# Kernel tuning notes

Hardware: AMD Instinct MI355X
Metric: run time of the kernel (lower is better)

## Reference

```python
import jax, jax.numpy as jnp
import numpy as np
import math

N_EMBD = 1024
N_HEAD = 16
BLOCK_SIZE = 2048
B, T = 4, 2048

def setup_inputs() -> dict:
    key = jax.random.key(0)
    ks = jax.random.split(key, 5)
    s = 0.02
    x = jax.random.normal(ks[0], (B, T, N_EMBD), dtype=jnp.float32)
    W_attn = jax.random.normal(ks[1], (N_EMBD, 3 * N_EMBD), dtype=jnp.float32) * s
    b_attn = jnp.zeros((3 * N_EMBD,), dtype=jnp.float32)
    W_proj = jax.random.normal(ks[2], (N_EMBD, N_EMBD), dtype=jnp.float32) * s
    b_proj = jnp.zeros((N_EMBD,), dtype=jnp.float32)
    return {"x": x, "W_attn": W_attn, "b_attn": b_attn, "W_proj": W_proj, "b_proj": b_proj}

def reference(x, W_attn, b_attn, W_proj, b_proj):
    b, t, c = x.shape
    hd = c // N_HEAD  # head dim
    qkv = x @ W_attn + b_attn                      # [B,T,3C]
    q, k, v = jnp.split(qkv, 3, axis=-1)
    # [B,T,C] -> [B,H,T,hd]
    q = q.reshape(b, t, N_HEAD, hd).transpose(0, 2, 1, 3)
    k = k.reshape(b, t, N_HEAD, hd).transpose(0, 2, 1, 3)
    v = v.reshape(b, t, N_HEAD, hd).transpose(0, 2, 1, 3)
    att = jnp.einsum('bhqd,bhkd->bhqk', q, k) * (1.0 / math.sqrt(hd))
    causal = jnp.tril(jnp.ones((t, t), dtype=bool))
    att = jnp.where(causal[None, None], att, -jnp.inf)
    att = jax.nn.softmax(att, axis=-1)
    y = jnp.einsum('bhqk,bhkd->bhqd', att, v)      # [B,H,T,hd]
    y = y.transpose(0, 2, 1, 3).reshape(b, t, c)
    return y @ W_proj + b_proj
```

## Files before the change

kernel.cpp:

```cpp
#include <hip/hip_runtime.h>

typedef unsigned short u16;
typedef __bf16 bf16x8 __attribute__((ext_vector_type(8)));
typedef float    f32x4 __attribute__((ext_vector_type(4)));
typedef unsigned short u16x8 __attribute__((ext_vector_type(8)));

__device__ __forceinline__ float bf2f(u16 v){ return __uint_as_float(((unsigned int)v) << 16); }
__device__ __forceinline__ u16 f2bf(float f){
    unsigned int u = __float_as_uint(f);
    u += 0x7fffu + ((u >> 16) & 1u);
    return (u16)(u >> 16);
}
__device__ __forceinline__ u16 f2bf_t(float f){ return (u16)(__float_as_uint(f) >> 16); }
__device__ __forceinline__ unsigned pack_trunc(float hi, float lo){
    return __builtin_amdgcn_perm(__float_as_uint(hi), __float_as_uint(lo), 0x07060302);
}
__device__ __forceinline__ float exp2_fast(float x){
    float r; asm("v_exp_f32 %0, %1" : "=v"(r) : "v"(x)); return r;
}

__device__ __forceinline__ void glds16(const u16* gp, u16* lp){
    __builtin_amdgcn_global_load_lds((unsigned int __attribute__((address_space(1)))*)gp,
                                     (unsigned int __attribute__((address_space(3)))*)lp,
                                     16, 0, 0);
}

__device__ __forceinline__ int probe_f32(const u16* __restrict__ xp){
    u16 lo = xp[2 * (threadIdx.x & 63)];
    int e = (lo >> 7) & 0xff;
    bool bad = !(e == 0 || (e > 96 && e < 160));
    return __popcll(__ballot(bad)) > 16;
}

__global__ __launch_bounds__(256) void conv_x(const void* __restrict__ src, u16* __restrict__ dst,
                                              const u16* __restrict__ xprobe){
    const int isf32 = probe_f32(xprobe);
    size_t i = ((size_t)blockIdx.x * 256 + threadIdx.x) * 8;
    if (isf32){
        const float* p = (const float*)src + i;
        float4 a = *(const float4*)p, b = *(const float4*)(p + 4);
        u16x8 o = { f2bf(a.x), f2bf(a.y), f2bf(a.z), f2bf(a.w),
                    f2bf(b.x), f2bf(b.y), f2bf(b.z), f2bf(b.w) };
        *(u16x8*)(dst + i) = o;
    } else {
        *(u16x8*)(dst + i) = *(const u16x8*)((const u16*)src + i);
    }
}

__global__ __launch_bounds__(256) void transposeW(const void* __restrict__ in, u16* __restrict__ out,
                                                  int R, int C, const u16* __restrict__ xprobe){
    __shared__ u16 t[64][65];
    const int isf32 = probe_f32(xprobe);
    const int c0 = blockIdx.x * 64, r0 = blockIdx.y * 64;
    const int tx = threadIdx.x & 15, ty = threadIdx.x >> 4;
#pragma unroll
    for (int i = 0; i < 4; i++){
        int r = ty + i * 16;
        u16 a, b, c, d;
        if (isf32){
            float4 v = *(const float4*)((const float*)in + (size_t)(r0 + r) * C + c0 + tx * 4);
            a = f2bf(v.x); b = f2bf(v.y); c = f2bf(v.z); d = f2bf(v.w);
        } else {
            ushort4 v = *(const ushort4*)((const u16*)in + (size_t)(r0 + r) * C + c0 + tx * 4);
            a = v.x; b = v.y; c = v.z; d = v.w;
        }
        t[r][tx*4+0] = a; t[r][tx*4+1] = b; t[r][tx*4+2] = c; t[r][tx*4+3] = d;
    }
    __syncthreads();
#pragma unroll
    for (int i = 0; i < 4; i++){
        int oc = ty + i * 16;
        ushort4 v;
        v.x = t[tx*4+0][oc]; v.y = t[tx*4+1][oc]; v.z = t[tx*4+2][oc]; v.w = t[tx*4+3][oc];
        *(ushort4*)(out + (size_t)(c0 + oc) * R + r0 + tx * 4) = v;
    }
}

#define CTS 136
template<int MODE>
__global__ __launch_bounds__(256) void gemm128(
    const u16* __restrict__ A, const u16* __restrict__ Bt, const void* __restrict__ bias,
    void* __restrict__ C, u16* __restrict__ Cq, u16* __restrict__ Ck, u16* __restrict__ Cv,
    const u16* __restrict__ xprobe, int M, int N, int K)
{
    __shared__ u16 lds[17408];
    u16* Asm = lds;
    u16* Bsm = lds + 8192;
    u16* Ct  = lds;
    const int isf32 = probe_f32(xprobe);
    const int tid = threadIdx.x;
    const int wave = tid >> 6, lane = tid & 63;
    const int quad = lane >> 4, ml = lane & 15;

    const int nbx = gridDim.x;
    int flat = blockIdx.y * nbx + blockIdx.x;
    const int cpx = (nbx * gridDim.y) >> 3;
    flat = (flat & 7) * cpx + (flat >> 3);
    const int m_blk = (flat / nbx) * 128;
    const int n_blk = (flat % nbx) * 128;

    const int wm = (wave >> 1) * 64, wn = (wave & 1) * 64;
    const int srow = lane >> 3;
    const int sch  = lane & 7;

    f32x4 acc[4][4];
#pragma unroll
    for (int a = 0; a < 4; a++)
#pragma unroll
        for (int b = 0; b < 4; b++)
            acc[a][b] = (f32x4){0.f, 0.f, 0.f, 0.f};

    for (int k0 = 0; k0 < K; k0 += 64){
        __syncthreads();
#pragma unroll
        for (int i = 0; i < 4; i++){
            int row = wave * 32 + i * 8 + srow;
            int sc  = sch ^ (row & 7);
            glds16(A  + (size_t)(m_blk + row) * K + k0 + sc * 8, Asm + (wave * 32 + i * 8) * 64);
            glds16(Bt + (size_t)(n_blk + row) * K + k0 + sc * 8, Bsm + (wave * 32 + i * 8) * 64);
        }
        __syncthreads();
#pragma unroll
        for (int ks = 0; ks < 2; ks++){
            bf16x8 af[4], bfr[4];
#pragma unroll
            for (int mt = 0; mt < 4; mt++)
                af[mt]  = *(const bf16x8*)&Asm[(wm + mt * 16 + ml) * 64 + ((ks * 4 + quad) ^ (ml & 7)) * 8];
#pragma unroll
            for (int nt = 0; nt < 4; nt++)
                bfr[nt] = *(const bf16x8*)&Bsm[(wn + nt * 16 + ml) * 64 + ((ks * 4 + quad) ^ (ml & 7)) * 8];
#pragma unroll
            for (int mt = 0; mt < 4; mt++)
#pragma unroll
                for (int nt = 0; nt < 4; nt++)
                    acc[mt][nt] = __builtin_amdgcn_mfma_f32_16x16x32_bf16(af[mt], bfr[nt], acc[mt][nt], 0, 0, 0);
        }
    }
    __syncthreads();

    const float QSC = 0.18033688f;
    if (MODE == 0){
        const int which = n_blk >> 10;
        const int hbase = (n_blk >> 6) & 15;
        if (which < 2){
            const float sc = (which == 0) ? QSC : 1.0f;
#pragma unroll
            for (int nt = 0; nt < 4; nt++){
                int col = wn + nt * 16 + ml;
                float bv = isf32 ? ((const float*)bias)[n_blk + col] : bf2f(((const u16*)bias)[n_blk + col]);
#pragma unroll
                for (int mt = 0; mt < 4; mt++){
                    int row0 = wm + mt * 16 + quad * 4;
#pragma unroll
                    for (int r = 0; r < 4; r++)
                        Ct[(row0 + r) * CTS + col] = f2bf_t((acc[mt][nt][r] + bv) * sc);
                }
            }
            __syncthreads();
            u16* dst0 = (which == 0) ? Cq : Ck;
            const int b = m_blk >> 11, t0 = m_blk & 2047;
#pragma unroll
            for (int i = 0; i < 8; i++){
                int u = i * 256 + tid;
                int row = u >> 4, c8 = u & 15;
                int h = hbase + (c8 >> 3), d8 = (c8 & 7) * 8;
                u16x8 v = *(const u16x8*)&Ct[row * CTS + c8 * 8];
                *(u16x8*)&dst0[(((size_t)(b * 16 + h)) * 2048 + (t0 + row)) * 64 + d8] = v;
            }
        } else {
#pragma unroll
            for (int nt = 0; nt < 4; nt++){
                int col = wn + nt * 16 + ml;
                float bv = isf32 ? ((const float*)bias)[n_blk + col] : bf2f(((const u16*)bias)[n_blk + col]);
#pragma unroll
                for (int mt = 0; mt < 4; mt++){
                    int row0 = wm + mt * 16 + quad * 4;
                    uint2 pk;
                    pk.x = pack_trunc(acc[mt][nt][1] + bv, acc[mt][nt][0] + bv);
                    pk.y = pack_trunc(acc[mt][nt][3] + bv, acc[mt][nt][2] + bv);
                    *(uint2*)&Ct[col * CTS + row0] = pk;
                }
            }
            __syncthreads();
            const int b = m_blk >> 11, t0 = m_blk & 2047;
#pragma unroll
            for (int i = 0; i < 8; i++){
                int u = i * 256 + tid;
                int col = u >> 4, c8 = u & 15;
                int h = hbase + (col >> 6), d = col & 63;
                u16x8 v = *(const u16x8*)&Ct[col * CTS + c8 * 8];
                *(u16x8*)&Cv[(((size_t)(b * 16 + h)) * 64 + d) * 2048 + t0 + c8 * 8] = v;
            }
        }
    } else {
#pragma unroll
        for (int nt = 0; nt < 4; nt++){
            int col = n_blk + wn + nt * 16 + ml;
            float bv = isf32 ? ((const float*)bias)[col] : bf2f(((const u16*)bias)[col]);
#pragma unroll
            for (int mt = 0; mt < 4; mt++){
                float o0 = acc[mt][nt][0] + bv, o1 = acc[mt][nt][1] + bv;
                float o2 = acc[mt][nt][2] + bv, o3 = acc[mt][nt][3] + bv;
                int row0 = m_blk + wm + mt * 16 + quad * 4;
                if (isf32){
                    float* p = (float*)C + (size_t)row0 * N + col;
                    p[0] = o0; p[N] = o1; p[2*N] = o2; p[3*N] = o3;
                } else {
                    u16* p = (u16*)C + (size_t)row0 * N + col;
                    p[0] = f2bf(o0); p[N] = f2bf(o1); p[2*N] = f2bf(o2); p[3*N] = f2bf(o3);
                }
            }
        }
    }
}

#define PS 136
__global__ __launch_bounds__(256) void attn_kernel(
    const u16* __restrict__ Q, const u16* __restrict__ K, const u16* __restrict__ Vt,
    u16* __restrict__ Y)
{
    __shared__ u16 Ksm[128 * 64];
    __shared__ u16 Vsm[64 * 128];
    __shared__ u16 Psm[4][32 * PS];

    const int tid = threadIdx.x, wave = tid >> 6, lane = tid & 63;
    const int quad = lane >> 4, ml = lane & 15;
    const int flat = blockIdx.x;
    const int qb = 15 - (flat >> 6);
    const int rest = flat & 63;
    const int bh = ((rest & 7) << 3) | (rest >> 3);
    const int q0 = qb * 128;
    const size_t base = (size_t)bh * (2048 * 64);
    const float NEG = -1.0e30f;

    bf16x8 qf[2][2];
#pragma unroll
    for (int mt = 0; mt < 2; mt++)
#pragma unroll
        for (int ks = 0; ks < 2; ks++)
            qf[mt][ks] = *(const bf16x8*)(Q + base + (size_t)(q0 + mt * 64 + wave * 16 + ml) * 64 + ks * 32 + quad * 8);

    f32x4 acc[2][4];
#pragma unroll
    for (int mt = 0; mt < 2; mt++)
#pragma unroll
        for (int nt = 0; nt < 4; nt++) acc[mt][nt] = (f32x4){0.f, 0.f, 0.f, 0.f};
    float l[2][4];
#pragma unroll
    for (int mt = 0; mt < 2; mt++)
#pragma unroll
        for (int r = 0; r < 4; r++) l[mt][r] = 0.f;

    const int ntj = qb + 1;
    for (int j = 0; j < ntj; j++){
        const int j0 = j * 128;
        __syncthreads();
#pragma unroll
        for (int i = 0; i < 4; i++){
            int ub = i * 256 + wave * 64;
            int u = ub + lane;
            int row = u >> 3, cg = (lane & 7) ^ (row & 7);
            glds16(K + base + (size_t)(j0 + row) * 64 + cg * 8, Ksm + ub * 8);
            int d = u >> 4, vg = (lane & 15) ^ (d & 15);
            glds16(Vt + base + (size_t)d * 2048 + j0 + vg * 8, Vsm + ub * 8);
        }
        __syncthreads();
        const bool lastj = (j == ntj - 1);

#pragma unroll
        for (int nt = 0; nt < 8; nt++){
            bf16x8 bk0 = *(const bf16x8*)&Ksm[(nt * 16 + ml) * 64 + ((quad)     ^ (ml & 7)) * 8];
            bf16x8 bk1 = *(const bf16x8*)&Ksm[(nt * 16 + ml) * 64 + ((4 + quad) ^ (ml & 7)) * 8];
            f32x4 z = {0.f, 0.f, 0.f, 0.f};
            f32x4 s0 = __builtin_amdgcn_mfma_f32_16x16x32_bf16(qf[0][0], bk0, z, 0, 0, 0);
            s0 = __builtin_amdgcn_mfma_f32_16x16x32_bf16(qf[0][1], bk1, s0, 0, 0, 0);
            f32x4 s1 = __builtin_amdgcn_mfma_f32_16x16x32_bf16(qf[1][0], bk0, z, 0, 0, 0);
            s1 = __builtin_amdgcn_mfma_f32_16x16x32_bf16(qf[1][1], bk1, s1, 0, 0, 0);
            if (lastj){
                int cl = nt * 16 + ml;
                int r0 = wave * 16 + quad * 4;
#pragma unroll
                for (int r = 0; r < 4; r++){
                    if (cl > r0 + r)      s0[r] = NEG;
                    if (cl > 64 + r0 + r) s1[r] = NEG;
                }
            }
#pragma unroll
            for (int r = 0; r < 4; r++){
                float p0 = exp2_fast(s0[r]); l[0][r] += p0;
                Psm[wave][(quad * 4 + r) * PS + nt * 16 + ml] = f2bf_t(p0);
                float p1 = exp2_fast(s1[r]); l[1][r] += p1;
                Psm[wave][(16 + quad * 4 + r) * PS + nt * 16 + ml] = f2bf_t(p1);
            }
        }
#pragma unroll
        for (int ks = 0; ks < 4; ks++){
            bf16x8 pf0 = *(const bf16x8*)&Psm[wave][ml * PS + ks * 32 + quad * 8];
            bf16x8 pf1 = *(const bf16x8*)&Psm[wave][(16 + ml) * PS + ks * 32 + quad * 8];
#pragma unroll
            for (int nt = 0; nt < 4; nt++){
                bf16x8 vf = *(const bf16x8*)&Vsm[(nt * 16 + ml) * 128 + (((ks * 4 + quad) ^ ml) & 15) * 8];
                acc[0][nt] = __builtin_amdgcn_mfma_f32_16x16x32_bf16(pf0, vf, acc[0][nt], 0, 0, 0);
                acc[1][nt] = __builtin_amdgcn_mfma_f32_16x16x32_bf16(pf1, vf, acc[1][nt], 0, 0, 0);
            }
        }
    }
    const int b = bh >> 4, h = bh & 15;
#pragma unroll
    for (int mt = 0; mt < 2; mt++){
        f32x4 inv;
#pragma unroll
        for (int r = 0; r < 4; r++){
            float t = l[mt][r];
            t += __shfl_xor(t, 1, 64);
            t += __shfl_xor(t, 2, 64);
            t += __shfl_xor(t, 4, 64);
            t += __shfl_xor(t, 8, 64);
            inv[r] = 1.0f / t;
        }
#pragma unroll
        for (int nt = 0; nt < 4; nt++)
#pragma unroll
            for (int r = 0; r < 4; r++){
                size_t row = (size_t)b * 2048 + q0 + mt * 64 + wave * 16 + quad * 4 + r;
                Y[row * 1024 + h * 64 + nt * 16 + ml] = f2bf(acc[mt][nt][r] * inv[r]);
            }
    }
}

extern "C" void kernel_launch(void* const* d_in, const int* in_sizes, int n_in,
                              void* d_out, int out_size, void* d_ws, size_t ws_size,
                              hipStream_t stream) {
    const void* x      = d_in[0];
    const void* W_attn = d_in[1];
    const void* b_attn = d_in[2];
    const void* W_proj = d_in[3];
    const void* b_proj = d_in[4];
    const u16* xprobe = (const u16*)x;

    u16* ws = (u16*)d_ws;
    u16* Qw = ws;
    u16* Kw = ws + 8u * 1024 * 1024;
    u16* Vw = ws + 16u * 1024 * 1024;
    u16* R  = ws + 24u * 1024 * 1024;
    u16* Wt_attn = R;
    u16* Yw      = R;
    u16* Wt_proj = Qw;
    u16* xb = (u16*)d_out;

    conv_x<<<4096, 256, 0, stream>>>(x, xb, xprobe);
    transposeW<<<dim3(48, 16), 256, 0, stream>>>(W_attn, Wt_attn, 1024, 3072, xprobe);
    gemm128<0><<<dim3(24, 64), 256, 0, stream>>>(
        xb, Wt_attn, b_attn, nullptr, Qw, Kw, Vw, xprobe, 8192, 3072, 1024);
    attn_kernel<<<1024, 256, 0, stream>>>(Qw, Kw, Vw, Yw);
    transposeW<<<dim3(16, 16), 256, 0, stream>>>(W_proj, Wt_proj, 1024, 1024, xprobe);
    gemm128<1><<<dim3(8, 64), 256, 0, stream>>>(
        Yw, Wt_proj, b_proj, d_out, nullptr, nullptr, nullptr, xprobe, 8192, 1024, 1024);
}
```

Measured before the change: 251.5 us.

## Triple-buffer GEMM LDS staging with async global-to-LDS prefetch

```diff
diff --git a/kernel.cpp b/kernel.cpp
--- a/kernel.cpp
+++ b/kernel.cpp
@@ -77,17 +77,19 @@
 }
 
 #define CTS 136
+#define BAR()    asm volatile("s_barrier" ::: "memory")
+#define WAITV(n) asm volatile("s_waitcnt vmcnt(" #n ")" ::: "memory")
+
 template<int MODE>
 __global__ __launch_bounds__(256) void gemm128(
     const u16* __restrict__ A, const u16* __restrict__ Bt, const void* __restrict__ bias,
     void* __restrict__ C, u16* __restrict__ Cq, u16* __restrict__ Ck, u16* __restrict__ Cv,
     const u16* __restrict__ xprobe, int M, int N, int K)
 {
-    __shared__ u16 lds[17408];
-    u16* Asm = lds;
-    u16* Bsm = lds + 8192;
-    u16* Ct  = lds;
+    __shared__ u16 lds[24576];
+    u16* Ct = lds;
     const int isf32 = probe_f32(xprobe);
+    WAITV(0);
     const int tid = threadIdx.x;
     const int wave = tid >> 6, lane = tid & 63;
     const int quad = lane >> 4, ml = lane & 15;
@@ -100,8 +102,23 @@
     const int n_blk = (flat % nbx) * 128;
 
     const int wm = (wave >> 1) * 64, wn = (wave & 1) * 64;
-    const int srow = lane >> 3;
-    const int sch  = lane & 7;
+
+    const int srow = tid >> 2;
+    const int csrc = (tid & 3) ^ ((tid >> 3) & 3);
+    const u16* pa0 = A  + (size_t)(m_blk + srow) * K + csrc * 8;
+    const u16* pa1 = pa0 + (size_t)64 * K;
+    const u16* pb0 = Bt + (size_t)(n_blk + srow) * K + csrc * 8;
+    const u16* pb1 = pb0 + (size_t)64 * K;
+
+    const int cread = (quad ^ ((ml >> 1) & 3)) * 8;
+
+    u16* s0 = lds; u16* s1 = lds + 8192; u16* s2 = lds + 16384;
+
+#define STAGE(sl, kt) { const size_t ko_ = (size_t)(kt) * 32;            \
+    glds16(pa0 + ko_, (sl) + wave * 512);                                \
+    glds16(pa1 + ko_, (sl) + 2048 + wave * 512);                         \
+    glds16(pb0 + ko_, (sl) + 4096 + wave * 512);                         \
+    glds16(pb1 + ko_, (sl) + 6144 + wave * 512); }
 
     f32x4 acc[4][4];
 #pragma unroll
@@ -110,32 +127,30 @@
         for (int b = 0; b < 4; b++)
             acc[a][b] = (f32x4){0.f, 0.f, 0.f, 0.f};
 
-    for (int k0 = 0; k0 < K; k0 += 64){
-        __syncthreads();
-#pragma unroll
-        for (int i = 0; i < 4; i++){
-            int row = wave * 32 + i * 8 + srow;
-            int sc  = sch ^ (row & 7);
-            glds16(A  + (size_t)(m_blk + row) * K + k0 + sc * 8, Asm + (wave * 32 + i * 8) * 64);
-            glds16(Bt + (size_t)(n_blk + row) * K + k0 + sc * 8, Bsm + (wave * 32 + i * 8) * 64);
-        }
-        __syncthreads();
-#pragma unroll
-        for (int ks = 0; ks < 2; ks++){
-            bf16x8 af[4], bfr[4];
-#pragma unroll
-            for (int mt = 0; mt < 4; mt++)
-                af[mt]  = *(const bf16x8*)&Asm[(wm + mt * 16 + ml) * 64 + ((ks * 4 + quad) ^ (ml & 7)) * 8];
+    const int T = K >> 5;
+    STAGE(s0, 0); STAGE(s1, 1);
+    WAITV(4);
+    BAR();
+
+    for (int t = 0; t < T; ++t){
+        if (t + 2 < T) STAGE(s2, t + 2);
+        bf16x8 af[4], bfr[4];
+#pragma unroll
+        for (int mt = 0; mt < 4; mt++)
+            af[mt]  = *(const bf16x8*)&s0[(wm + mt * 16 + ml) * 32 + cread];
+#pragma unroll
+        for (int nt = 0; nt < 4; nt++)
+            bfr[nt] = *(const bf16x8*)&s0[4096 + (wn + nt * 16 + ml) * 32 + cread];
+#pragma unroll
+        for (int mt = 0; mt < 4; mt++)
 #pragma unroll
             for (int nt = 0; nt < 4; nt++)
-                bfr[nt] = *(const bf16x8*)&Bsm[(wn + nt * 16 + ml) * 64 + ((ks * 4 + quad) ^ (ml & 7)) * 8];
-#pragma unroll
-            for (int mt = 0; mt < 4; mt++)
-#pragma unroll
-                for (int nt = 0; nt < 4; nt++)
-                    acc[mt][nt] = __builtin_amdgcn_mfma_f32_16x16x32_bf16(af[mt], bfr[nt], acc[mt][nt], 0, 0, 0);
-        }
-    }
+                acc[mt][nt] = __builtin_amdgcn_mfma_f32_16x16x32_bf16(af[mt], bfr[nt], acc[mt][nt], 0, 0, 0);
+        if (t < T - 2) { WAITV(4); } else { WAITV(0); }
+        BAR();
+        u16* tmp = s0; s0 = s1; s1 = s2; s2 = tmp;
+    }
+#undef STAGE
     __syncthreads();
 
     const float QSC = 0.18033688f;
```

Result: no change. 250.5 us (-0.4%).
